# Kernel tuning notes

Measured on AMD Instinct MI355X. Metric: run time of the kernel, lower is better.

## Reference

```python
import jax, jax.numpy as jnp
import numpy as np

WS = 8
NH = 6
LF_DIM = 64
HF_DIM = 192
HEAD_DIM = HF_DIM // NH


def _rpb_index(ws):
    # static numpy computation of the relative-position index, (N, N) int
    coords = np.stack(np.meshgrid(np.arange(ws), np.arange(ws), indexing='ij')).reshape(2, -1)
    rel = coords[:, :, None] - coords[:, None, :]          # (2, N, N)
    rel = rel.transpose(1, 2, 0).astype(np.int64)          # (N, N, 2)
    rel[..., 0] += ws - 1
    rel[..., 1] += ws - 1
    rel[..., 0] *= 2 * ws - 1
    return rel.sum(-1)                                     # (N, N)

_RPB_IDX = _rpb_index(WS)


def _layernorm(x, g, b, eps=1e-5):
    mu = jnp.mean(x, axis=-1, keepdims=True)
    var = jnp.mean(jnp.square(x - mu), axis=-1, keepdims=True)
    return (x - mu) * jax.lax.rsqrt(var + eps) * g + b


def _window_partition(x, ws):
    # (B, C, H, W) -> (B*nH*nW, ws*ws, C)
    B, C, H, W = x.shape
    x = x.reshape(B, C, H // ws, ws, W // ws, ws)
    x = x.transpose(0, 2, 4, 3, 5, 1)                      # B nH nW ws ws C
    return x.reshape(-1, ws * ws, C)


def _window_reverse(wins, ws, H, W):
    # (B*nH*nW, ws*ws, C) -> (B, C, H, W)
    nH, nW = H // ws, W // ws
    B = wins.shape[0] // (nH * nW)
    C = wins.shape[-1]
    x = wins.reshape(B, nH, nW, ws, ws, C)
    x = x.transpose(0, 5, 1, 3, 2, 4)                      # B C nH ws nW ws
    return x.reshape(B, C, H, W)


def setup_inputs() -> dict:
    key = jax.random.key(0)
    ks = jax.random.split(key, 16)
    B, H, W = 4, 256, 256
    s = 0.02
    return {
        'y_lf': jax.random.normal(ks[0], (B, LF_DIM, H, W), jnp.float32),
        'y_hf': jax.random.normal(ks[1], (B, HF_DIM, H, W), jnp.float32),
        'norm_lf_g': jnp.ones((LF_DIM,), jnp.float32),
        'norm_lf_b': jnp.zeros((LF_DIM,), jnp.float32),
        'norm_hf_g': jnp.ones((HF_DIM,), jnp.float32),
        'norm_hf_b': jnp.zeros((HF_DIM,), jnp.float32),
        'Wq': jax.random.normal(ks[2], (LF_DIM, HF_DIM), jnp.float32) * s,
        'bq': jnp.zeros((HF_DIM,), jnp.float32),
        'Wk': jax.random.normal(ks[3], (HF_DIM, HF_DIM), jnp.float32) * s,
        'bk': jnp.zeros((HF_DIM,), jnp.float32),
        'Wv': jax.random.normal(ks[4], (HF_DIM, HF_DIM), jnp.float32) * s,
        'bv': jnp.zeros((HF_DIM,), jnp.float32),
        'Wo': jax.random.normal(ks[5], (HF_DIM, HF_DIM), jnp.float32) * s,
        'bo': jnp.zeros((HF_DIM,), jnp.float32),
        'rpb_table': jax.random.normal(ks[6], ((2 * WS - 1) ** 2, NH), jnp.float32) * s,
    }


def reference(y_lf, y_hf, norm_lf_g, norm_lf_b, norm_hf_g, norm_hf_b,
              Wq, bq, Wk, bk, Wv, bv, Wo, bo, rpb_table):
    B, _, H, W = y_lf.shape
    ws, N = WS, WS * WS
    # H, W chosen divisible by ws so the reflect-pad in the original is a no-op
    lf_w = _window_partition(y_lf, ws)                     # (bw, N, C_lf)
    hf_w = _window_partition(y_hf, ws)                     # (bw, N, C_hf)
    hf_residual = hf_w
    lf_n = _layernorm(lf_w, norm_lf_g, norm_lf_b)
    hf_n = _layernorm(hf_w, norm_hf_g, norm_hf_b)
    bw = lf_w.shape[0]
    Q = (lf_n @ Wq + bq).reshape(bw, N, NH, HEAD_DIM).transpose(0, 2, 1, 3)
    K = (hf_n @ Wk + bk).reshape(bw, N, NH, HEAD_DIM).transpose(0, 2, 1, 3)
    V = (hf_n @ Wv + bv).reshape(bw, N, NH, HEAD_DIM).transpose(0, 2, 1, 3)
    scale = HEAD_DIM ** -0.5
    attn = jnp.einsum('bhnd,bhmd->bhnm', Q, K) * scale     # (bw, h, N, N)
    bias = rpb_table[_RPB_IDX.reshape(-1)].reshape(N, N, NH).transpose(2, 0, 1)
    attn = jax.nn.softmax(attn + bias[None], axis=-1)
    out = jnp.einsum('bhnm,bhmd->bhnd', attn, V)
    out = out.transpose(0, 2, 1, 3).reshape(bw, N, HF_DIM)
    out = out @ Wo + bo + hf_residual
    return _window_reverse(out, ws, H, W)                  # (B, C_hf, H, W)
```

## Files before the change

kernel.cpp:

```cpp
#include <hip/hip_runtime.h>
#include <cstdint>
#include <cstddef>

#define DEVI __device__ __forceinline__

typedef __bf16 bf16x8 __attribute__((ext_vector_type(8)));
typedef float  floatx4 __attribute__((ext_vector_type(4)));

constexpr int NHEAD = 6;
constexpr int CLF = 64, CHF = 192;
constexpr int IMG = 256;
constexpr int HW  = IMG * IMG;

constexpr int OFF_WKV = 0;
constexpr int OFF_WO  = 24576;
constexpr int OFF_KP  = 36864;
constexpr int OFF_VT  = 45056;
constexpr int OFF_RPB = 49152;
constexpr int SMEM_BYTES = 51856;

constexpr int LOFF_HF  = 0;
constexpr int LOFF_LF  = 25600;
constexpr int LOFF_RED = 34816;
constexpr int P_HFL = 200, P_LFL = 72;
constexpr int P_WQ = 72;

DEVI unsigned short f2b(float f) {
  unsigned u = __float_as_uint(f);
  u += 0x7fffu + ((u >> 16) & 1u);
  return (unsigned short)(u >> 16);
}
DEVI float b2f(unsigned short s) { return __uint_as_float(((unsigned)s) << 16); }

DEVI floatx4 mfma_bf16(bf16x8 a, bf16x8 b, floatx4 c) {
  return __builtin_amdgcn_mfma_f32_16x16x32_bf16(a, b, c, 0, 0, 0);
}

DEVI int swz8(int row, int off) { return off ^ ((row & 7) << 3); }
DEVI int swz4(int row, int off) { return off ^ ((row & 3) << 3); }

__global__ void wca_prep(const float* __restrict__ Wq, const float* __restrict__ Wk,
                         const float* __restrict__ Wv, const float* __restrict__ Wo,
                         unsigned short* __restrict__ wT) {
  int i = blockIdx.x * 256 + threadIdx.x;
  if (i < 12288) {
    int n = i >> 6, k = i & 63;
    wT[i] = f2b(Wq[k * 192 + n]);
  } else if (i < 49152) {
    int j = i - 12288, n = j / 192, k = j - n * 192;
    wT[i] = f2b(Wk[k * 192 + n]);
  } else if (i < 86016) {
    int j = i - 49152, n = j / 192, k = j - n * 192;
    wT[i] = f2b(Wv[k * 192 + n]);
  } else {
    int j = i - 86016, n = j / 192, k = j - n * 192;
    wT[i] = f2b(Wo[k * 192 + n]);
  }
}

__global__ __launch_bounds__(256, 2) void wca_main(
    const float* __restrict__ ylf, const float* __restrict__ yhf,
    const float* __restrict__ glf, const float* __restrict__ blf,
    const float* __restrict__ ghf, const float* __restrict__ bhf,
    const float* __restrict__ bq,  const float* __restrict__ bk,
    const float* __restrict__ bv,  const float* __restrict__ bo,
    const float* __restrict__ rpb, const unsigned short* __restrict__ wT,
    float* __restrict__ out) {
  __shared__ __align__(16) char smem[SMEM_BYTES];
  unsigned short* s_wkv = (unsigned short*)(smem + OFF_WKV);
  unsigned short* s_wo  = (unsigned short*)(smem + OFF_WO);
  unsigned short* s_kp  = (unsigned short*)(smem + OFF_KP);
  unsigned short* s_vt  = (unsigned short*)(smem + OFF_VT);
  unsigned short* s_rpb = (unsigned short*)(smem + OFF_RPB);
  unsigned short* s_hfL = (unsigned short*)(smem + LOFF_HF);
  unsigned short* s_lfL = (unsigned short*)(smem + LOFF_LF);
  float* s_red = (float*)(smem + LOFF_RED);
  unsigned short* s_wq = (unsigned short*)(smem);

  const int tid  = threadIdx.x;
  const int lane = tid & 63;
  const int wv   = tid >> 6;
  const int quad = lane >> 4;
  const int l16  = lane & 15;

  const int g   = blockIdx.x;
  const int wid = ((g & 7) << 9) | (g >> 3);
  const int b   = wid >> 10;
  const int wy  = (wid >> 5) & 31;
  const int wx  = wid & 31;
  const int h0  = wy << 3, w0 = wx << 3;

  const int t_own = tid & 63;
  const int cg    = tid >> 6;
  const int ty    = t_own >> 3, tx = t_own & 7;

  float lfv[16], hfv[48];
  float ls = 0.f, l2 = 0.f, hs = 0.f, h2 = 0.f;
  {
    const float* p = ylf + ((size_t)(b * CLF + cg * 16) * IMG + (h0 + ty)) * IMG + (w0 + tx);
#pragma unroll
    for (int k = 0; k < 16; k++) {
      float v = p[(size_t)k * HW];
      lfv[k] = v; ls += v; l2 += v * v;
    }
  }
  {
    const float* p = yhf + ((size_t)(b * CHF + cg * 48) * IMG + (h0 + ty)) * IMG + (w0 + tx);
#pragma unroll
    for (int k = 0; k < 48; k++) {
      float v = p[(size_t)k * HW];
      hfv[k] = v; hs += v; h2 += v * v;
    }
  }
  s_red[0 * 256 + (cg << 6) + t_own] = ls;
  s_red[1 * 256 + (cg << 6) + t_own] = l2;
  s_red[2 * 256 + (cg << 6) + t_own] = hs;
  s_red[3 * 256 + (cg << 6) + t_own] = h2;
  __syncthreads();
  float su = 0.f, sq = 0.f, hu = 0.f, hq = 0.f;
#pragma unroll
  for (int gg = 0; gg < 4; gg++) {
    su += s_red[0 * 256 + (gg << 6) + t_own];
    sq += s_red[1 * 256 + (gg << 6) + t_own];
    hu += s_red[2 * 256 + (gg << 6) + t_own];
    hq += s_red[3 * 256 + (gg << 6) + t_own];
  }
  const float mu_lf = su * (1.f / 64.f);
  const float rs_lf = rsqrtf(sq * (1.f / 64.f) - mu_lf * mu_lf + 1e-5f);
  const float mu_hf = hu * (1.f / 192.f);
  const float rs_hf = rsqrtf(hq * (1.f / 192.f) - mu_hf * mu_hf + 1e-5f);

#pragma unroll
  for (int j = 0; j < 4; j++) {
    uint64_t w = 0;
#pragma unroll
    for (int m = 0; m < 4; m++) {
      int c = cg * 16 + j * 4 + m;
      float v = (lfv[j * 4 + m] - mu_lf) * rs_lf * glf[c] + blf[c];
      w |= (uint64_t)f2b(v) << (16 * m);
    }
    *(uint64_t*)(s_lfL + t_own * P_LFL + cg * 16 + j * 4) = w;
  }
#pragma unroll
  for (int j = 0; j < 12; j++) {
    uint64_t w = 0;
#pragma unroll
    for (int m = 0; m < 4; m++) {
      int c = cg * 48 + j * 4 + m;
      float v = (hfv[j * 4 + m] - mu_hf) * rs_hf * ghf[c] + bhf[c];
      w |= (uint64_t)f2b(v) << (16 * m);
    }
    *(uint64_t*)(s_hfL + t_own * P_HFL + cg * 48 + j * 4) = w;
  }
  __syncthreads();

  bf16x8 lfr0 = *(const bf16x8*)(s_lfL + (wv * 16 + l16) * P_LFL + quad * 8);
  bf16x8 lfr1 = *(const bf16x8*)(s_lfL + (wv * 16 + l16) * P_LFL + 32 + quad * 8);
  bf16x8 hfr[6];
#pragma unroll
  for (int ks = 0; ks < 6; ks++)
    hfr[ks] = *(const bf16x8*)(s_hfL + (wv * 16 + l16) * P_HFL + ks * 32 + quad * 8);
  __syncthreads();

  const unsigned short* wqT = wT;
  const unsigned short* wkT = wT + 12288;
  const unsigned short* wvT = wT + 49152;
  const unsigned short* woT = wT + 86016;

#pragma unroll
  for (int i = 0; i < 6; i++) {
    int p = i * 256 + tid;
    int n = p >> 3, sub = p & 7;
    *(uint4*)(s_wq + n * P_WQ + sub * 8) = *(const uint4*)(wqT + n * 64 + sub * 8);
  }
  for (int i = tid; i < 225 * NHEAD; i += 256) s_rpb[i] = f2b(rpb[i]);
  __syncthreads();

  const int rowbase = wv * 16 + quad * 4;

  bf16x8 aq[NHEAD];
#pragma unroll
  for (int h = 0; h < NHEAD; h++) {
#pragma unroll
    for (int nt = 0; nt < 2; nt++) {
      const int n = h * 32 + nt * 16 + l16;
      floatx4 acc = {0.f, 0.f, 0.f, 0.f};
      acc = mfma_bf16(lfr0, *(const bf16x8*)(s_wq + n * P_WQ + quad * 8), acc);
      acc = mfma_bf16(lfr1, *(const bf16x8*)(s_wq + n * P_WQ + 32 + quad * 8), acc);
      const float bqv = bq[n];
#pragma unroll
      for (int r = 0; r < 4; r++)
        s_kp[(rowbase + r) * 64 + swz8(rowbase + r, nt * 16 + l16)] = f2b(acc[r] + bqv);
    }
    aq[h] = *(const bf16x8*)(s_kp + (wv * 16 + l16) * 64 + swz8(wv * 16 + l16, quad * 8));
  }
  __syncthreads();

  auto stageKV = [&](int h) {
    const unsigned short* sk = wkT + h * 6144;
    const unsigned short* sv = wvT + h * 6144;
#pragma unroll
    for (int i = 0; i < 3; i++) {
      int p = i * 256 + tid;
      int nl = p / 24, sub = p - nl * 24;
      *(uint4*)(s_wkv + nl * 192 + swz8(nl, sub * 8)) =
          *(const uint4*)(sk + nl * 192 + sub * 8);
      *(uint4*)(s_wkv + (32 + nl) * 192 + swz8(32 + nl, sub * 8)) =
          *(const uint4*)(sv + nl * 192 + sub * 8);
    }
  };

  stageKV(0);
  __syncthreads();

  floatx4 oa[12];
  const floatx4 zero = {0.f, 0.f, 0.f, 0.f};
#pragma unroll
  for (int ct = 0; ct < 12; ct++) oa[ct] = zero;

#pragma unroll
  for (int h = 0; h < NHEAD; h++) {
#pragma unroll
    for (int nt = 0; nt < 2; nt++) {
      const int n = h * 32 + nt * 16 + l16;
      const int nl = nt * 16 + l16;
      floatx4 acc = {0.f, 0.f, 0.f, 0.f};
#pragma unroll
      for (int ks = 0; ks < 6; ks++)
        acc = mfma_bf16(hfr[ks],
            *(const bf16x8*)(s_wkv + nl * 192 + swz8(nl, ks * 32 + quad * 8)), acc);
      const float bkv = bk[n];
#pragma unroll
      for (int r = 0; r < 4; r++)
        s_kp[(rowbase + r) * 64 + swz8(rowbase + r, nt * 16 + l16)] = f2b(acc[r] + bkv);
    }
#pragma unroll
    for (int nt = 0; nt < 2; nt++) {
      const int n = h * 32 + nt * 16 + l16;
      const int nl = nt * 16 + l16;
      floatx4 acc = {0.f, 0.f, 0.f, 0.f};
#pragma unroll
      for (int ks = 0; ks < 6; ks++)
        acc = mfma_bf16(hfr[ks],
            *(const bf16x8*)(s_wkv + (32 + nl) * 192 + swz8(32 + nl, ks * 32 + quad * 8)), acc);
      const float bvv = bv[n];
#pragma unroll
      for (int r = 0; r < 4; r++)
        s_vt[nl * 64 + swz8(nl, rowbase + r)] = f2b(acc[r] + bvv);
    }
    __syncthreads();

#pragma unroll
    for (int i = 0; i < 3; i++) {
      int p = i * 256 + tid;
      int n = p >> 2, sub = p & 3;
      *(uint4*)(s_wo + n * 32 + swz4(n, sub * 8)) =
          *(const uint4*)(woT + n * 192 + h * 32 + sub * 8);
    }
    if (h + 1 < NHEAD) stageKV(h + 1);

    float sv[4][4];
#pragma unroll
    for (int ct = 0; ct < 4; ct++) {
      bf16x8 kb = *(const bf16x8*)(s_kp + (ct * 16 + l16) * 64 + swz8(ct * 16 + l16, quad * 8));
      floatx4 acc = {0.f, 0.f, 0.f, 0.f};
      acc = mfma_bf16(aq[h], kb, acc);
#pragma unroll
      for (int r = 0; r < 4; r++) {
        int row = rowbase + r, col = ct * 16 + l16;
        int dy = (row >> 3) - (col >> 3) + 7;
        int dx = (row & 7) - (col & 7) + 7;
        sv[ct][r] = acc[r] * 0.17677669529663688f + b2f(s_rpb[(dy * 15 + dx) * NHEAD + h]);
      }
    }
#pragma unroll
    for (int r = 0; r < 4; r++) {
      float m = fmaxf(fmaxf(sv[0][r], sv[1][r]), fmaxf(sv[2][r], sv[3][r]));
      m = fmaxf(m, __shfl_xor(m, 1));
      m = fmaxf(m, __shfl_xor(m, 2));
      m = fmaxf(m, __shfl_xor(m, 4));
      m = fmaxf(m, __shfl_xor(m, 8));
      const float L2E = 1.4426950408889634f;
      float e0 = exp2f((sv[0][r] - m) * L2E);
      float e1 = exp2f((sv[1][r] - m) * L2E);
      float e2 = exp2f((sv[2][r] - m) * L2E);
      float e3 = exp2f((sv[3][r] - m) * L2E);
      float s = e0 + e1 + e2 + e3;
      s += __shfl_xor(s, 1);
      s += __shfl_xor(s, 2);
      s += __shfl_xor(s, 4);
      s += __shfl_xor(s, 8);
      float inv = 1.f / s;
      sv[0][r] = e0 * inv; sv[1][r] = e1 * inv; sv[2][r] = e2 * inv; sv[3][r] = e3 * inv;
    }
    __syncthreads();

#pragma unroll
    for (int ct = 0; ct < 4; ct++)
#pragma unroll
      for (int r = 0; r < 4; r++)
        s_kp[(rowbase + r) * 64 + swz8(rowbase + r, ct * 16 + l16)] = f2b(sv[ct][r]);

    floatx4 pv0 = {0.f, 0.f, 0.f, 0.f}, pv1 = {0.f, 0.f, 0.f, 0.f};
#pragma unroll
    for (int ks = 0; ks < 2; ks++) {
      bf16x8 pa = *(const bf16x8*)(s_kp + (wv * 16 + l16) * 64 + swz8(wv * 16 + l16, ks * 32 + quad * 8));
      pv0 = mfma_bf16(pa, *(const bf16x8*)(s_vt + l16 * 64 + swz8(l16, ks * 32 + quad * 8)), pv0);
      pv1 = mfma_bf16(pa, *(const bf16x8*)(s_vt + (16 + l16) * 64 + swz8(16 + l16, ks * 32 + quad * 8)), pv1);
    }
#pragma unroll
    for (int r = 0; r < 4; r++) {
      s_kp[(rowbase + r) * 64 + swz8(rowbase + r, l16)]      = f2b(pv0[r]);
      s_kp[(rowbase + r) * 64 + swz8(rowbase + r, 16 + l16)] = f2b(pv1[r]);
    }
    bf16x8 aoh = *(const bf16x8*)(s_kp + (wv * 16 + l16) * 64 + swz8(wv * 16 + l16, quad * 8));
    __syncthreads();

#pragma unroll
    for (int ct = 0; ct < 12; ct++) {
      bf16x8 bb = *(const bf16x8*)(s_wo + (ct * 16 + l16) * 32 + swz4(ct * 16 + l16, quad * 8));
      oa[ct] = mfma_bf16(aoh, bb, oa[ct]);
    }
  }
  __syncthreads();

  unsigned short* s_ostg = (unsigned short*)(smem);
#pragma unroll
  for (int ct = 0; ct < 12; ct++) {
    const int col = ct * 16 + l16;
    const float bov = bo[col];
#pragma unroll
    for (int r = 0; r < 4; r++)
      s_ostg[(rowbase + r) * 200 + col] = f2b(oa[ct][r] + bov);
  }
  __syncthreads();

#pragma unroll
  for (int k = 0; k < 12; k++) {
    int chunk = k * 256 + tid;
    int c   = chunk >> 4;
    int sub = chunk & 15;
    int yy  = sub >> 1;
    int x4  = (sub & 1) << 2;
    int t0  = (yy << 3) + x4;
    size_t gidx = ((size_t)(b * CHF + c) * IMG + (h0 + yy)) * IMG + w0 + x4;
    float4 res = *(const float4*)(yhf + gidx);
    float4 v;
    v.x = b2f(s_ostg[(t0 + 0) * 200 + c]) + res.x;
    v.y = b2f(s_ostg[(t0 + 1) * 200 + c]) + res.y;
    v.z = b2f(s_ostg[(t0 + 2) * 200 + c]) + res.z;
    v.w = b2f(s_ostg[(t0 + 3) * 200 + c]) + res.w;
    *(float4*)(out + gidx) = v;
  }
}

extern "C" void kernel_launch(void* const* d_in, const int* in_sizes, int n_in,
                              void* d_out, int out_size, void* d_ws, size_t ws_size,
                              hipStream_t stream) {
  const float* ylf = (const float*)d_in[0];
  const float* yhf = (const float*)d_in[1];
  const float* glf = (const float*)d_in[2];
  const float* blf = (const float*)d_in[3];
  const float* ghf = (const float*)d_in[4];
  const float* bhf = (const float*)d_in[5];
  const float* Wq  = (const float*)d_in[6];
  const float* bq  = (const float*)d_in[7];
  const float* Wk  = (const float*)d_in[8];
  const float* bk  = (const float*)d_in[9];
  const float* Wv  = (const float*)d_in[10];
  const float* bv  = (const float*)d_in[11];
  const float* Wo  = (const float*)d_in[12];
  const float* bo  = (const float*)d_in[13];
  const float* rpb = (const float*)d_in[14];
  unsigned short* wT = (unsigned short*)d_ws;

  wca_prep<<<480, 256, 0, stream>>>(Wq, Wk, Wv, Wo, wT);
  wca_main<<<4096, 256, 0, stream>>>(ylf, yhf, glf, blf, ghf, bhf,
                                     bq, bk, bv, bo, rpb, wT, (float*)d_out);
}
```

Before: 644.1 us.

## Compute full K/V projections up front and batch output projection per window

Restructures the per-head loop: K and V for all heads are now projected in three 64-column weight stages each and stored in shared memory, and the attention loop per head then needs no block-wide barriers, using per-wave scratch for Q and P tiles. The output projection is moved out of the head loop into three staged 64-column GEMMs over the full 192-wide attention output, replacing twelve per-head accumulators. This aims to cut __syncthreads count and register pressure, at the cost of raising shared memory from about 52KB to about 81KB, which may limit occupancy below the two blocks per CU requested.

```diff
diff --git a/kernel.cpp b/kernel.cpp
--- a/kernel.cpp
+++ b/kernel.cpp
@@ -12,18 +12,14 @@
 constexpr int IMG = 256;
 constexpr int HW  = IMG * IMG;
 
-constexpr int OFF_WKV = 0;
-constexpr int OFF_WO  = 24576;
-constexpr int OFF_KP  = 36864;
-constexpr int OFF_VT  = 45056;
-constexpr int OFF_RPB = 49152;
-constexpr int SMEM_BYTES = 51856;
-
-constexpr int LOFF_HF  = 0;
-constexpr int LOFF_LF  = 25600;
-constexpr int LOFF_RED = 34816;
-constexpr int P_HFL = 200, P_LFL = 72;
-constexpr int P_WQ = 72;
+constexpr int OFF_KA  = 0;
+constexpr int OFF_VT  = 24576;
+constexpr int OFF_ST  = 49152;
+constexpr int OFF_PW  = 73728;
+constexpr int OFF_RPB = 78848;
+constexpr int SMEM_BYTES = 81552;
+constexpr int LOFF_LF  = 24576;
+constexpr int LOFF_RED = 33792;
 
 DEVI unsigned short f2b(float f) {
   unsigned u = __float_as_uint(f);
@@ -37,7 +33,6 @@
 }
 
 DEVI int swz8(int row, int off) { return off ^ ((row & 7) << 3); }
-DEVI int swz4(int row, int off) { return off ^ ((row & 3) << 3); }
 
 __global__ void wca_prep(const float* __restrict__ Wq, const float* __restrict__ Wk,
                          const float* __restrict__ Wv, const float* __restrict__ Wo,
@@ -67,21 +62,19 @@
     const float* __restrict__ rpb, const unsigned short* __restrict__ wT,
     float* __restrict__ out) {
   __shared__ __align__(16) char smem[SMEM_BYTES];
-  unsigned short* s_wkv = (unsigned short*)(smem + OFF_WKV);
-  unsigned short* s_wo  = (unsigned short*)(smem + OFF_WO);
-  unsigned short* s_kp  = (unsigned short*)(smem + OFF_KP);
+  unsigned short* s_ka  = (unsigned short*)(smem + OFF_KA);
   unsigned short* s_vt  = (unsigned short*)(smem + OFF_VT);
+  unsigned short* s_st  = (unsigned short*)(smem + OFF_ST);
   unsigned short* s_rpb = (unsigned short*)(smem + OFF_RPB);
-  unsigned short* s_hfL = (unsigned short*)(smem + LOFF_HF);
   unsigned short* s_lfL = (unsigned short*)(smem + LOFF_LF);
   float* s_red = (float*)(smem + LOFF_RED);
-  unsigned short* s_wq = (unsigned short*)(smem);
 
   const int tid  = threadIdx.x;
   const int lane = tid & 63;
   const int wv   = tid >> 6;
   const int quad = lane >> 4;
   const int l16  = lane & 15;
+  unsigned short* s_pw = (unsigned short*)(smem + OFF_PW) + wv * 640;
 
   const int g   = blockIdx.x;
   const int wid = ((g & 7) << 9) | (g >> 3);
@@ -139,7 +132,7 @@
       float v = (lfv[j * 4 + m] - mu_lf) * rs_lf * glf[c] + blf[c];
       w |= (uint64_t)f2b(v) << (16 * m);
     }
-    *(uint64_t*)(s_lfL + t_own * P_LFL + cg * 16 + j * 4) = w;
+    *(uint64_t*)(s_lfL + t_own * 72 + cg * 16 + j * 4) = w;
   }
 #pragma unroll
   for (int j = 0; j < 12; j++) {
@@ -150,33 +143,33 @@
       float v = (hfv[j * 4 + m] - mu_hf) * rs_hf * ghf[c] + bhf[c];
       w |= (uint64_t)f2b(v) << (16 * m);
     }
-    *(uint64_t*)(s_hfL + t_own * P_HFL + cg * 48 + j * 4) = w;
-  }
-  __syncthreads();
-
-  bf16x8 lfr0 = *(const bf16x8*)(s_lfL + (wv * 16 + l16) * P_LFL + quad * 8);
-  bf16x8 lfr1 = *(const bf16x8*)(s_lfL + (wv * 16 + l16) * P_LFL + 32 + quad * 8);
+    *(uint64_t*)(s_ka + t_own * 192 + swz8(t_own, cg * 48 + j * 4)) = w;
+  }
+  __syncthreads();
+
+  const int myrow = wv * 16 + l16;
+  bf16x8 lfr0 = *(const bf16x8*)(s_lfL + myrow * 72 + quad * 8);
+  bf16x8 lfr1 = *(const bf16x8*)(s_lfL + myrow * 72 + 32 + quad * 8);
   bf16x8 hfr[6];
 #pragma unroll
   for (int ks = 0; ks < 6; ks++)
-    hfr[ks] = *(const bf16x8*)(s_hfL + (wv * 16 + l16) * P_HFL + ks * 32 + quad * 8);
+    hfr[ks] = *(const bf16x8*)(s_ka + myrow * 192 + swz8(myrow, ks * 32 + quad * 8));
   __syncthreads();
 
   const unsigned short* wqT = wT;
   const unsigned short* wkT = wT + 12288;
   const unsigned short* wvT = wT + 49152;
   const unsigned short* woT = wT + 86016;
+  const int rowbase = wv * 16 + quad * 4;
 
 #pragma unroll
   for (int i = 0; i < 6; i++) {
     int p = i * 256 + tid;
     int n = p >> 3, sub = p & 7;
-    *(uint4*)(s_wq + n * P_WQ + sub * 8) = *(const uint4*)(wqT + n * 64 + sub * 8);
+    *(uint4*)(s_st + n * 64 + swz8(n, sub * 8)) = *(const uint4*)(wqT + n * 64 + sub * 8);
   }
   for (int i = tid; i < 225 * NHEAD; i += 256) s_rpb[i] = f2b(rpb[i]);
   __syncthreads();
-
-  const int rowbase = wv * 16 + quad * 4;
 
   bf16x8 aq[NHEAD];
 #pragma unroll
@@ -185,89 +178,86 @@
     for (int nt = 0; nt < 2; nt++) {
       const int n = h * 32 + nt * 16 + l16;
       floatx4 acc = {0.f, 0.f, 0.f, 0.f};
-      acc = mfma_bf16(lfr0, *(const bf16x8*)(s_wq + n * P_WQ + quad * 8), acc);
-      acc = mfma_bf16(lfr1, *(const bf16x8*)(s_wq + n * P_WQ + 32 + quad * 8), acc);
+      acc = mfma_bf16(lfr0, *(const bf16x8*)(s_st + n * 64 + swz8(n, quad * 8)), acc);
+      acc = mfma_bf16(lfr1, *(const bf16x8*)(s_st + n * 64 + swz8(n, 32 + quad * 8)), acc);
       const float bqv = bq[n];
 #pragma unroll
       for (int r = 0; r < 4; r++)
-        s_kp[(rowbase + r) * 64 + swz8(rowbase + r, nt * 16 + l16)] = f2b(acc[r] + bqv);
-    }
-    aq[h] = *(const bf16x8*)(s_kp + (wv * 16 + l16) * 64 + swz8(wv * 16 + l16, quad * 8));
-  }
-  __syncthreads();
-
-  auto stageKV = [&](int h) {
-    const unsigned short* sk = wkT + h * 6144;
-    const unsigned short* sv = wvT + h * 6144;
-#pragma unroll
-    for (int i = 0; i < 3; i++) {
+        s_pw[(quad * 4 + r) * 40 + nt * 16 + l16] = f2b(acc[r] + bqv);
+    }
+    aq[h] = *(const bf16x8*)(s_pw + l16 * 40 + quad * 8);
+  }
+  __syncthreads();
+
+  auto stageThird = [&](const unsigned short* src) {
+#pragma unroll
+    for (int i = 0; i < 6; i++) {
       int p = i * 256 + tid;
       int nl = p / 24, sub = p - nl * 24;
-      *(uint4*)(s_wkv + nl * 192 + swz8(nl, sub * 8)) =
-          *(const uint4*)(sk + nl * 192 + sub * 8);
-      *(uint4*)(s_wkv + (32 + nl) * 192 + swz8(32 + nl, sub * 8)) =
-          *(const uint4*)(sv + nl * 192 + sub * 8);
+      *(uint4*)(s_st + nl * 192 + swz8(nl, sub * 8)) =
+          *(const uint4*)(src + nl * 192 + sub * 8);
     }
   };
 
-  stageKV(0);
-  __syncthreads();
-
-  floatx4 oa[12];
-  const floatx4 zero = {0.f, 0.f, 0.f, 0.f};
-#pragma unroll
-  for (int ct = 0; ct < 12; ct++) oa[ct] = zero;
+#pragma unroll
+  for (int t = 0; t < 3; t++) {
+    stageThird(wkT + t * 64 * 192);
+    __syncthreads();
+#pragma unroll
+    for (int hh = 0; hh < 2; hh++) {
+#pragma unroll
+      for (int nt = 0; nt < 2; nt++) {
+        const int nl = hh * 32 + nt * 16 + l16;
+        const int n  = t * 64 + nl;
+        floatx4 acc = {0.f, 0.f, 0.f, 0.f};
+#pragma unroll
+        for (int ks = 0; ks < 6; ks++)
+          acc = mfma_bf16(hfr[ks],
+              *(const bf16x8*)(s_st + nl * 192 + swz8(nl, ks * 32 + quad * 8)), acc);
+        const float bkv = bk[n];
+#pragma unroll
+        for (int r = 0; r < 4; r++)
+          s_ka[(rowbase + r) * 192 + swz8(rowbase + r, n)] = f2b(acc[r] + bkv);
+      }
+    }
+    __syncthreads();
+  }
+#pragma unroll
+  for (int t = 0; t < 3; t++) {
+    stageThird(wvT + t * 64 * 192);
+    __syncthreads();
+#pragma unroll
+    for (int hh = 0; hh < 2; hh++) {
+#pragma unroll
+      for (int nt = 0; nt < 2; nt++) {
+        const int nl = hh * 32 + nt * 16 + l16;
+        const int n  = t * 64 + nl;
+        floatx4 acc = {0.f, 0.f, 0.f, 0.f};
+#pragma unroll
+        for (int ks = 0; ks < 6; ks++)
+          acc = mfma_bf16(hfr[ks],
+              *(const bf16x8*)(s_st + nl * 192 + swz8(nl, ks * 32 + quad * 8)), acc);
+        const float bvv = bv[n];
+#pragma unroll
+        for (int r = 0; r < 4; r++)
+          s_vt[n * 64 + swz8(n, rowbase + r)] = f2b(acc[r] + bvv);
+      }
+    }
+    __syncthreads();
+  }
 
 #pragma unroll
   for (int h = 0; h < NHEAD; h++) {
-#pragma unroll
-    for (int nt = 0; nt < 2; nt++) {
-      const int n = h * 32 + nt * 16 + l16;
-      const int nl = nt * 16 + l16;
-      floatx4 acc = {0.f, 0.f, 0.f, 0.f};
-#pragma unroll
-      for (int ks = 0; ks < 6; ks++)
-        acc = mfma_bf16(hfr[ks],
-            *(const bf16x8*)(s_wkv + nl * 192 + swz8(nl, ks * 32 + quad * 8)), acc);
-      const float bkv = bk[n];
-#pragma unroll
-      for (int r = 0; r < 4; r++)
-        s_kp[(rowbase + r) * 64 + swz8(rowbase + r, nt * 16 + l16)] = f2b(acc[r] + bkv);
-    }
-#pragma unroll
-    for (int nt = 0; nt < 2; nt++) {
-      const int n = h * 32 + nt * 16 + l16;
-      const int nl = nt * 16 + l16;
-      floatx4 acc = {0.f, 0.f, 0.f, 0.f};
-#pragma unroll
-      for (int ks = 0; ks < 6; ks++)
-        acc = mfma_bf16(hfr[ks],
-            *(const bf16x8*)(s_wkv + (32 + nl) * 192 + swz8(32 + nl, ks * 32 + quad * 8)), acc);
-      const float bvv = bv[n];
-#pragma unroll
-      for (int r = 0; r < 4; r++)
-        s_vt[nl * 64 + swz8(nl, rowbase + r)] = f2b(acc[r] + bvv);
-    }
-    __syncthreads();
-
-#pragma unroll
-    for (int i = 0; i < 3; i++) {
-      int p = i * 256 + tid;
-      int n = p >> 2, sub = p & 3;
-      *(uint4*)(s_wo + n * 32 + swz4(n, sub * 8)) =
-          *(const uint4*)(woT + n * 192 + h * 32 + sub * 8);
-    }
-    if (h + 1 < NHEAD) stageKV(h + 1);
-
     float sv[4][4];
 #pragma unroll
     for (int ct = 0; ct < 4; ct++) {
-      bf16x8 kb = *(const bf16x8*)(s_kp + (ct * 16 + l16) * 64 + swz8(ct * 16 + l16, quad * 8));
+      const int kr = ct * 16 + l16;
+      bf16x8 kb = *(const bf16x8*)(s_ka + kr * 192 + swz8(kr, h * 32 + quad * 8));
       floatx4 acc = {0.f, 0.f, 0.f, 0.f};
       acc = mfma_bf16(aq[h], kb, acc);
 #pragma unroll
       for (int r = 0; r < 4; r++) {
-        int row = rowbase + r, col = ct * 16 + l16;
+        int row = rowbase + r, col = kr;
         int dy = (row >> 3) - (col >> 3) + 7;
         int dx = (row & 7) - (col & 7) + 7;
         sv[ct][r] = acc[r] * 0.17677669529663688f + b2f(s_rpb[(dy * 15 + dx) * NHEAD + h]);
@@ -293,48 +283,60 @@
       float inv = 1.f / s;
       sv[0][r] = e0 * inv; sv[1][r] = e1 * inv; sv[2][r] = e2 * inv; sv[3][r] = e3 * inv;
     }
-    __syncthreads();
-
-#pragma unroll
-    for (int ct = 0; ct < 4; ct++)
+    floatx4 pv0 = {0.f, 0.f, 0.f, 0.f}, pv1 = {0.f, 0.f, 0.f, 0.f};
+#pragma unroll
+    for (int ks = 0; ks < 2; ks++) {
+#pragma unroll
+      for (int r = 0; r < 4; r++) {
+        s_pw[(quad * 4 + r) * 40 + l16]      = f2b(sv[ks * 2 + 0][r]);
+        s_pw[(quad * 4 + r) * 40 + 16 + l16] = f2b(sv[ks * 2 + 1][r]);
+      }
+      bf16x8 pa = *(const bf16x8*)(s_pw + l16 * 40 + quad * 8);
+      const int d0 = h * 32 + l16, d1 = h * 32 + 16 + l16;
+      pv0 = mfma_bf16(pa, *(const bf16x8*)(s_vt + d0 * 64 + swz8(d0, ks * 32 + quad * 8)), pv0);
+      pv1 = mfma_bf16(pa, *(const bf16x8*)(s_vt + d1 * 64 + swz8(d1, ks * 32 + quad * 8)), pv1);
+    }
+#pragma unroll
+    for (int r = 0; r < 4; r++) {
+      const int row = rowbase + r;
+      s_st[row * 192 + swz8(row, h * 32 + l16)]      = f2b(pv0[r]);
+      s_st[row * 192 + swz8(row, h * 32 + 16 + l16)] = f2b(pv1[r]);
+    }
+  }
+  __syncthreads();
+
+  bf16x8 aoh[6];
+#pragma unroll
+  for (int ks = 0; ks < 6; ks++)
+    aoh[ks] = *(const bf16x8*)(s_st + myrow * 192 + swz8(myrow, ks * 32 + quad * 8));
+#pragma unroll
+  for (int t = 0; t < 3; t++) {
+#pragma unroll
+    for (int i = 0; i < 6; i++) {
+      int p = i * 256 + tid;
+      int nl = p / 24, sub = p - nl * 24;
+      *(uint4*)(s_ka + nl * 192 + swz8(nl, sub * 8)) =
+          *(const uint4*)(woT + (t * 64 + nl) * 192 + sub * 8);
+    }
+    __syncthreads();
+#pragma unroll
+    for (int c4 = 0; c4 < 4; c4++) {
+      const int nl = c4 * 16 + l16;
+      floatx4 acc = {0.f, 0.f, 0.f, 0.f};
+#pragma unroll
+      for (int ks = 0; ks < 6; ks++)
+        acc = mfma_bf16(aoh[ks],
+            *(const bf16x8*)(s_ka + nl * 192 + swz8(nl, ks * 32 + quad * 8)), acc);
+      const int col = t * 64 + c4 * 16 + l16;
+      const float bov = bo[col];
 #pragma unroll
       for (int r = 0; r < 4; r++)
-        s_kp[(rowbase + r) * 64 + swz8(rowbase + r, ct * 16 + l16)] = f2b(sv[ct][r]);
-
-    floatx4 pv0 = {0.f, 0.f, 0.f, 0.f}, pv1 = {0.f, 0.f, 0.f, 0.f};
-#pragma unroll
-    for (int ks = 0; ks < 2; ks++) {
-      bf16x8 pa = *(const bf16x8*)(s_kp + (wv * 16 + l16) * 64 + swz8(wv * 16 + l16, ks * 32 + quad * 8));
-      pv0 = mfma_bf16(pa, *(const bf16x8*)(s_vt + l16 * 64 + swz8(l16, ks * 32 + quad * 8)), pv0);
-      pv1 = mfma_bf16(pa, *(const bf16x8*)(s_vt + (16 + l16) * 64 + swz8(16 + l16, ks * 32 + quad * 8)), pv1);
-    }
-#pragma unroll
-    for (int r = 0; r < 4; r++) {
-      s_kp[(rowbase + r) * 64 + swz8(rowbase + r, l16)]      = f2b(pv0[r]);
-      s_kp[(rowbase + r) * 64 + swz8(rowbase + r, 16 + l16)] = f2b(pv1[r]);
-    }
-    bf16x8 aoh = *(const bf16x8*)(s_kp + (wv * 16 + l16) * 64 + swz8(wv * 16 + l16, quad * 8));
-    __syncthreads();
-
-#pragma unroll
-    for (int ct = 0; ct < 12; ct++) {
-      bf16x8 bb = *(const bf16x8*)(s_wo + (ct * 16 + l16) * 32 + swz4(ct * 16 + l16, quad * 8));
-      oa[ct] = mfma_bf16(aoh, bb, oa[ct]);
-    }
-  }
-  __syncthreads();
-
-  unsigned short* s_ostg = (unsigned short*)(smem);
-#pragma unroll
-  for (int ct = 0; ct < 12; ct++) {
-    const int col = ct * 16 + l16;
-    const float bov = bo[col];
-#pragma unroll
-    for (int r = 0; r < 4; r++)
-      s_ostg[(rowbase + r) * 200 + col] = f2b(oa[ct][r] + bov);
-  }
-  __syncthreads();
-
+        s_vt[(rowbase + r) * 192 + swz8(rowbase + r, col)] = f2b(acc[r] + bov);
+    }
+    __syncthreads();
+  }
+
+  unsigned short* s_os = s_vt;
 #pragma unroll
   for (int k = 0; k < 12; k++) {
     int chunk = k * 256 + tid;
@@ -346,10 +348,10 @@
     size_t gidx = ((size_t)(b * CHF + c) * IMG + (h0 + yy)) * IMG + w0 + x4;
     float4 res = *(const float4*)(yhf + gidx);
     float4 v;
-    v.x = b2f(s_ostg[(t0 + 0) * 200 + c]) + res.x;
-    v.y = b2f(s_ostg[(t0 + 1) * 200 + c]) + res.y;
-    v.z = b2f(s_ostg[(t0 + 2) * 200 + c]) + res.z;
-    v.w = b2f(s_ostg[(t0 + 3) * 200 + c]) + res.w;
+    v.x = b2f(s_os[(t0 + 0) * 192 + swz8(t0 + 0, c)]) + res.x;
+    v.y = b2f(s_os[(t0 + 1) * 192 + swz8(t0 + 1, c)]) + res.y;
+    v.z = b2f(s_os[(t0 + 2) * 192 + swz8(t0 + 2, c)]) + res.z;
+    v.w = b2f(s_os[(t0 + 3) * 192 + swz8(t0 + 3, c)]) + res.w;
     *(float4*)(out + gidx) = v;
   }
 }
```

Result: slower. 694.4 us (+7.8%).

## Use per-wave P scratch buffer, drop softmax max-subtraction and one barrier

Applied to the files above, without the earlier changes.

Adds a per-wave padded LDS scratch region for Q, P and the PV output so these wave-private round trips no longer share the K buffer. That removes one __syncthreads per head. The K/V projection MFMA chain is split into two independent accumulators to shorten the dependency chain. Softmax no longer subtracts the row max, which saves shuffles but risks overflow for large logits. LDS usage grows, which may affect the 2-block occupancy.

```diff
diff --git a/kernel.cpp b/kernel.cpp
--- a/kernel.cpp
+++ b/kernel.cpp
@@ -14,12 +14,13 @@
 
 constexpr int OFF_WKV = 0;
 constexpr int OFF_WO  = 24576;
-constexpr int OFF_KP  = 36864;
+constexpr int OFF_K   = 36864;
 constexpr int OFF_VT  = 45056;
-constexpr int OFF_RPB = 49152;
-constexpr int SMEM_BYTES = 51856;
-
-constexpr int LOFF_HF  = 0;
+constexpr int OFF_PW  = 49152;
+constexpr int OFF_RPB = 58368;
+constexpr int SMEM_BYTES = 61072;
+constexpr int P_PW = 72;
+
 constexpr int LOFF_LF  = 25600;
 constexpr int LOFF_RED = 34816;
 constexpr int P_HFL = 200, P_LFL = 72;
@@ -69,10 +70,10 @@
   __shared__ __align__(16) char smem[SMEM_BYTES];
   unsigned short* s_wkv = (unsigned short*)(smem + OFF_WKV);
   unsigned short* s_wo  = (unsigned short*)(smem + OFF_WO);
-  unsigned short* s_kp  = (unsigned short*)(smem + OFF_KP);
+  unsigned short* s_k   = (unsigned short*)(smem + OFF_K);
   unsigned short* s_vt  = (unsigned short*)(smem + OFF_VT);
   unsigned short* s_rpb = (unsigned short*)(smem + OFF_RPB);
-  unsigned short* s_hfL = (unsigned short*)(smem + LOFF_HF);
+  unsigned short* s_hfL = (unsigned short*)(smem);
   unsigned short* s_lfL = (unsigned short*)(smem + LOFF_LF);
   float* s_red = (float*)(smem + LOFF_RED);
   unsigned short* s_wq = (unsigned short*)(smem);
@@ -82,6 +83,7 @@
   const int wv   = tid >> 6;
   const int quad = lane >> 4;
   const int l16  = lane & 15;
+  unsigned short* s_pw = (unsigned short*)(smem + OFF_PW) + wv * 16 * P_PW;
 
   const int g   = blockIdx.x;
   const int wid = ((g & 7) << 9) | (g >> 3);
@@ -154,12 +156,13 @@
   }
   __syncthreads();
 
-  bf16x8 lfr0 = *(const bf16x8*)(s_lfL + (wv * 16 + l16) * P_LFL + quad * 8);
-  bf16x8 lfr1 = *(const bf16x8*)(s_lfL + (wv * 16 + l16) * P_LFL + 32 + quad * 8);
+  const int myrow = wv * 16 + l16;
+  bf16x8 lfr0 = *(const bf16x8*)(s_lfL + myrow * P_LFL + quad * 8);
+  bf16x8 lfr1 = *(const bf16x8*)(s_lfL + myrow * P_LFL + 32 + quad * 8);
   bf16x8 hfr[6];
 #pragma unroll
   for (int ks = 0; ks < 6; ks++)
-    hfr[ks] = *(const bf16x8*)(s_hfL + (wv * 16 + l16) * P_HFL + ks * 32 + quad * 8);
+    hfr[ks] = *(const bf16x8*)(s_hfL + myrow * P_HFL + ks * 32 + quad * 8);
   __syncthreads();
 
   const unsigned short* wqT = wT;
@@ -190,9 +193,9 @@
       const float bqv = bq[n];
 #pragma unroll
       for (int r = 0; r < 4; r++)
-        s_kp[(rowbase + r) * 64 + swz8(rowbase + r, nt * 16 + l16)] = f2b(acc[r] + bqv);
-    }
-    aq[h] = *(const bf16x8*)(s_kp + (wv * 16 + l16) * 64 + swz8(wv * 16 + l16, quad * 8));
+        s_pw[(quad * 4 + r) * P_PW + nt * 16 + l16] = f2b(acc[r] + bqv);
+    }
+    aq[h] = *(const bf16x8*)(s_pw + l16 * P_PW + quad * 8);
   }
   __syncthreads();
 
@@ -224,25 +227,33 @@
     for (int nt = 0; nt < 2; nt++) {
       const int n = h * 32 + nt * 16 + l16;
       const int nl = nt * 16 + l16;
-      floatx4 acc = {0.f, 0.f, 0.f, 0.f};
-#pragma unroll
-      for (int ks = 0; ks < 6; ks++)
-        acc = mfma_bf16(hfr[ks],
-            *(const bf16x8*)(s_wkv + nl * 192 + swz8(nl, ks * 32 + quad * 8)), acc);
+      floatx4 a0 = zero, a1 = zero;
+#pragma unroll
+      for (int ks = 0; ks < 3; ks++) {
+        a0 = mfma_bf16(hfr[ks],
+            *(const bf16x8*)(s_wkv + nl * 192 + swz8(nl, ks * 32 + quad * 8)), a0);
+        a1 = mfma_bf16(hfr[ks + 3],
+            *(const bf16x8*)(s_wkv + nl * 192 + swz8(nl, (ks + 3) * 32 + quad * 8)), a1);
+      }
+      floatx4 acc = a0 + a1;
       const float bkv = bk[n];
 #pragma unroll
       for (int r = 0; r < 4; r++)
-        s_kp[(rowbase + r) * 64 + swz8(rowbase + r, nt * 16 + l16)] = f2b(acc[r] + bkv);
+        s_k[(rowbase + r) * 64 + swz8(rowbase + r, nt * 16 + l16)] = f2b(acc[r] + bkv);
     }
 #pragma unroll
     for (int nt = 0; nt < 2; nt++) {
       const int n = h * 32 + nt * 16 + l16;
       const int nl = nt * 16 + l16;
-      floatx4 acc = {0.f, 0.f, 0.f, 0.f};
-#pragma unroll
-      for (int ks = 0; ks < 6; ks++)
-        acc = mfma_bf16(hfr[ks],
-            *(const bf16x8*)(s_wkv + (32 + nl) * 192 + swz8(32 + nl, ks * 32 + quad * 8)), acc);
+      floatx4 a0 = zero, a1 = zero;
+#pragma unroll
+      for (int ks = 0; ks < 3; ks++) {
+        a0 = mfma_bf16(hfr[ks],
+            *(const bf16x8*)(s_wkv + (32 + nl) * 192 + swz8(32 + nl, ks * 32 + quad * 8)), a0);
+        a1 = mfma_bf16(hfr[ks + 3],
+            *(const bf16x8*)(s_wkv + (32 + nl) * 192 + swz8(32 + nl, (ks + 3) * 32 + quad * 8)), a1);
+      }
+      floatx4 acc = a0 + a1;
       const float bvv = bv[n];
 #pragma unroll
       for (int r = 0; r < 4; r++)
@@ -262,12 +273,13 @@
     float sv[4][4];
 #pragma unroll
     for (int ct = 0; ct < 4; ct++) {
-      bf16x8 kb = *(const bf16x8*)(s_kp + (ct * 16 + l16) * 64 + swz8(ct * 16 + l16, quad * 8));
-      floatx4 acc = {0.f, 0.f, 0.f, 0.f};
+      const int kr = ct * 16 + l16;
+      bf16x8 kb = *(const bf16x8*)(s_k + kr * 64 + swz8(kr, quad * 8));
+      floatx4 acc = zero;
       acc = mfma_bf16(aq[h], kb, acc);
 #pragma unroll
       for (int r = 0; r < 4; r++) {
-        int row = rowbase + r, col = ct * 16 + l16;
+        int row = rowbase + r, col = kr;
         int dy = (row >> 3) - (col >> 3) + 7;
         int dx = (row & 7) - (col & 7) + 7;
         sv[ct][r] = acc[r] * 0.17677669529663688f + b2f(s_rpb[(dy * 15 + dx) * NHEAD + h]);
@@ -275,16 +287,11 @@
     }
 #pragma unroll
     for (int r = 0; r < 4; r++) {
-      float m = fmaxf(fmaxf(sv[0][r], sv[1][r]), fmaxf(sv[2][r], sv[3][r]));
-      m = fmaxf(m, __shfl_xor(m, 1));
-      m = fmaxf(m, __shfl_xor(m, 2));
-      m = fmaxf(m, __shfl_xor(m, 4));
-      m = fmaxf(m, __shfl_xor(m, 8));
       const float L2E = 1.4426950408889634f;
-      float e0 = exp2f((sv[0][r] - m) * L2E);
-      float e1 = exp2f((sv[1][r] - m) * L2E);
-      float e2 = exp2f((sv[2][r] - m) * L2E);
-      float e3 = exp2f((sv[3][r] - m) * L2E);
+      float e0 = exp2f(sv[0][r] * L2E);
+      float e1 = exp2f(sv[1][r] * L2E);
+      float e2 = exp2f(sv[2][r] * L2E);
+      float e3 = exp2f(sv[3][r] * L2E);
       float s = e0 + e1 + e2 + e3;
       s += __shfl_xor(s, 1);
       s += __shfl_xor(s, 2);
@@ -293,27 +300,25 @@
       float inv = 1.f / s;
       sv[0][r] = e0 * inv; sv[1][r] = e1 * inv; sv[2][r] = e2 * inv; sv[3][r] = e3 * inv;
     }
-    __syncthreads();
-
 #pragma unroll
     for (int ct = 0; ct < 4; ct++)
 #pragma unroll
       for (int r = 0; r < 4; r++)
-        s_kp[(rowbase + r) * 64 + swz8(rowbase + r, ct * 16 + l16)] = f2b(sv[ct][r]);
-
-    floatx4 pv0 = {0.f, 0.f, 0.f, 0.f}, pv1 = {0.f, 0.f, 0.f, 0.f};
+        s_pw[(quad * 4 + r) * P_PW + ct * 16 + l16] = f2b(sv[ct][r]);
+
+    floatx4 pv0 = zero, pv1 = zero;
 #pragma unroll
     for (int ks = 0; ks < 2; ks++) {
-      bf16x8 pa = *(const bf16x8*)(s_kp + (wv * 16 + l16) * 64 + swz8(wv * 16 + l16, ks * 32 + quad * 8));
+      bf16x8 pa = *(const bf16x8*)(s_pw + l16 * P_PW + ks * 32 + quad * 8);
       pv0 = mfma_bf16(pa, *(const bf16x8*)(s_vt + l16 * 64 + swz8(l16, ks * 32 + quad * 8)), pv0);
       pv1 = mfma_bf16(pa, *(const bf16x8*)(s_vt + (16 + l16) * 64 + swz8(16 + l16, ks * 32 + quad * 8)), pv1);
     }
 #pragma unroll
     for (int r = 0; r < 4; r++) {
-      s_kp[(rowbase + r) * 64 + swz8(rowbase + r, l16)]      = f2b(pv0[r]);
-      s_kp[(rowbase + r) * 64 + swz8(rowbase + r, 16 + l16)] = f2b(pv1[r]);
-    }
-    bf16x8 aoh = *(const bf16x8*)(s_kp + (wv * 16 + l16) * 64 + swz8(wv * 16 + l16, quad * 8));
+      s_pw[(quad * 4 + r) * P_PW + l16]      = f2b(pv0[r]);
+      s_pw[(quad * 4 + r) * P_PW + 16 + l16] = f2b(pv1[r]);
+    }
+    bf16x8 aoh = *(const bf16x8*)(s_pw + l16 * P_PW + quad * 8);
     __syncthreads();
 
 #pragma unroll
```

Result: faster. 627.0 us (median of 2 runs) (-2.7%).
